# Performance work log

Hardware: AMD Instinct MI355X
Metric: run time of the kernel (lower is better)

## Reference

```python
import jax, jax.numpy as jnp
from jax import lax
import numpy as np

STEP = 0.1            # step_size
INC = 1.5             # bracket_expansion_increase
MAX_EXPAND = 16       # fixed cap on bracket-expansion iterations (masked no-ops after convergence)
MAX_SHRINK = 24       # fixed cap on shrinkage-rejection iterations


def setup_inputs() -> dict:
    key = jax.random.key(0)
    kx, kw = jax.random.split(key)
    B, D = 65536, 128
    x = jax.random.normal(kx, (B, D), jnp.float32)
    W = jax.random.normal(kw, (D, D), jnp.float32) / np.float32(np.sqrt(D))
    return {"x": x, "W": W}


def _potential(x, W):
    # correlated Gaussian potential: -0.5 * ||W x||^2, per chain
    z = x @ W.T                      # [B, D]
    return -0.5 * jnp.sum(z * z, axis=-1)  # [B]


def _slice_sample(x, W):
    B = x.shape[0]
    key = jax.random.key(42)
    k_y, k_dir, k_u0, k_shr = jax.random.split(key, 4)

    pot = _potential(x, W)                               # [B]
    # y = log(1 - u) + potential  (log of uniform height under the density)
    y = jnp.log1p(-jax.random.uniform(k_y, pot.shape, jnp.float32)) + pot

    dirs = jax.random.normal(k_dir, x.shape, jnp.float32)
    dirs = dirs / jnp.linalg.norm(dirs, axis=-1, keepdims=True)  # unit slice directions

    mask0 = y < pot

    # --- bracket expansion (lower: sign=-1, upper: sign=+1), masked fixed-trip scan ---
    def expand(sign):
        def body(carry, i):
            b, mask = carry
            step_i = STEP * jnp.power(jnp.float32(INC), i.astype(jnp.float32))
            b = jnp.where(mask, b + sign * step_i, b)
            pot_b = _potential(x + b[:, None] * dirs, W)
            mask = mask & (y < pot_b)
            return (b, mask), None
        (b, _), _ = lax.scan(body, (jnp.zeros((B,), jnp.float32), mask0),
                             jnp.arange(MAX_EXPAND))
        return b

    lb = expand(-1.0)
    ub = expand(+1.0)

    # --- initial proposal on the bracket ---
    u = jax.random.uniform(k_u0, (B,), jnp.float32) * (ub - lb) + lb
    x_new = x + u[:, None] * dirs
    mask = _potential(x_new, W) < y   # rejected chains

    # --- shrinkage loop (masked fixed-trip scan) ---
    def shrink(carry, k):
        u, lb, ub, x_new, mask = carry
        smaller = u < 0
        lb = jnp.where(mask & smaller, u, lb)
        ub = jnp.where(mask & ~smaller, u, ub)
        u_prop = jax.random.uniform(k, (B,), jnp.float32) * (ub - lb) + lb
        u = jnp.where(mask, u_prop, u)
        cand = x + u[:, None] * dirs
        pot_c = _potential(cand, W)
        x_new = jnp.where(mask[:, None], cand, x_new)
        mask = mask & (pot_c < y)
        return (u, lb, ub, x_new, mask), None

    keys = jax.random.split(k_shr, MAX_SHRINK)
    (u, lb, ub, x_new, mask), _ = lax.scan(shrink, (u, lb, ub, x_new, mask), keys)
    return x_new


def reference(x, W):
    return _slice_sample(x, W)
```

## Files before the change

kernel.cpp:

```cpp
#include <hip/hip_runtime.h>
#include <stdint.h>
#include <math.h>


#define BD 128
#define NB 65536
#define WS 132
#define XDS 130

typedef float f32x2 __attribute__((ext_vector_type(2)));
typedef struct { f32x2 lo, hi; } f32x2x2;

#define PK_FMA_LO(acc, xd, wp) \
  asm("v_pk_fma_f32 %0, %1, %2, %0 op_sel_hi:[1,0,1]" \
      : "+v"(acc) : "v"(xd), "v"(wp))
#define PK_FMA_HI(acc, xd, wp) \
  asm("v_pk_fma_f32 %0, %1, %2, %0 op_sel:[0,1,0] op_sel_hi:[1,1,1]" \
      : "+v"(acc) : "v"(xd), "v"(wp))

__host__ __device__ inline uint32_t rotl32(uint32_t v, int s) {
  return (v << s) | (v >> (32 - s));
}

__host__ __device__ inline void tf2x32(uint32_t k0, uint32_t k1,
                                       uint32_t c0, uint32_t c1,
                                       uint32_t* o0, uint32_t* o1) {
  uint32_t ks2 = k0 ^ k1 ^ 0x1BD11BDAu;
  uint32_t x0 = c0 + k0, x1 = c1 + k1;
#define TFR(r) x0 += x1; x1 = rotl32(x1, (r)); x1 ^= x0;
  TFR(13) TFR(15) TFR(26) TFR(6)
  x0 += k1;  x1 += ks2 + 1u;
  TFR(17) TFR(29) TFR(16) TFR(24)
  x0 += ks2; x1 += k0 + 2u;
  TFR(13) TFR(15) TFR(26) TFR(6)
  x0 += k0;  x1 += k1 + 3u;
  TFR(17) TFR(29) TFR(16) TFR(24)
  x0 += k1;  x1 += ks2 + 4u;
  TFR(13) TFR(15) TFR(26) TFR(6)
  x0 += ks2; x1 += k0 + 5u;
#undef TFR
  *o0 = x0; *o1 = x1;
}

__device__ inline uint32_t jbits(uint32_t k0, uint32_t k1, uint32_t n) {
  uint32_t a, b;
  tf2x32(k0, k1, 0u, n, &a, &b);
  return a ^ b;
}

__device__ inline float u01(uint32_t bits) {
  return __fsub_rn(__uint_as_float((bits >> 9) | 0x3f800000u), 1.0f);
}

__device__ inline float xla_log1p(float x) {
  float u  = __fadd_rn(x, 1.0f);
  float lg = (float)log((double)u);
  float sm = __fmul_rn(__fadd_rn(__fmul_rn(-0.5f, x), 1.0f), x);
  return (fabsf(x) < 1e-4f) ? sm : lg;
}

__device__ inline float xla_erfinv(float x) {
  float xx = __fmul_rn(x, x);
  float w  = -xla_log1p(-xx);
  float p;
  if (w < 5.0f) {
    float ww = __fsub_rn(w, 2.5f);
    p = 2.81022636e-08f;
    p = __fadd_rn(3.43273939e-07f,  __fmul_rn(p, ww));
    p = __fadd_rn(-3.5233877e-06f,  __fmul_rn(p, ww));
    p = __fadd_rn(-4.39150654e-06f, __fmul_rn(p, ww));
    p = __fadd_rn(0.00021858087f,   __fmul_rn(p, ww));
    p = __fadd_rn(-0.00125372503f,  __fmul_rn(p, ww));
    p = __fadd_rn(-0.00417768164f,  __fmul_rn(p, ww));
    p = __fadd_rn(0.246640727f,     __fmul_rn(p, ww));
    p = __fadd_rn(1.50140941f,      __fmul_rn(p, ww));
  } else {
    float ww = __fsub_rn(__fsqrt_rn(w), 3.0f);
    p = -0.000200214257f;
    p = __fadd_rn(0.000100950558f,  __fmul_rn(p, ww));
    p = __fadd_rn(0.00134934322f,   __fmul_rn(p, ww));
    p = __fadd_rn(-0.00367342844f,  __fmul_rn(p, ww));
    p = __fadd_rn(0.00573950773f,   __fmul_rn(p, ww));
    p = __fadd_rn(-0.0076224613f,   __fmul_rn(p, ww));
    p = __fadd_rn(0.00943887047f,   __fmul_rn(p, ww));
    p = __fadd_rn(1.00167406f,      __fmul_rn(p, ww));
    p = __fadd_rn(2.83297682f,      __fmul_rn(p, ww));
  }
  return __fmul_rn(p, x);
}

__device__ __attribute__((always_inline)) inline float potential16(
    const f32x2* __restrict__ xdr, const float* __restrict__ wr, float coef) {
  float z[8] = {0.f, 0.f, 0.f, 0.f, 0.f, 0.f, 0.f, 0.f};
#pragma unroll 2
  for (int q = 0; q < 32; ++q) {
    float4 p01 = *(const float4*)(xdr + q * 4);
    float4 p23 = *(const float4*)(xdr + q * 4 + 2);
    float c0 = __fadd_rn(p01.x, __fmul_rn(coef, p01.y));
    float c1 = __fadd_rn(p01.z, __fmul_rn(coef, p01.w));
    float c2 = __fadd_rn(p23.x, __fmul_rn(coef, p23.y));
    float c3 = __fadd_rn(p23.z, __fmul_rn(coef, p23.w));
#pragma unroll
    for (int m = 0; m < 8; ++m) {
      float4 wv = *(const float4*)(wr + m * (16 * WS) + q * 4);
      z[m] = __fmaf_rn(c0, wv.x, z[m]);
      z[m] = __fmaf_rn(c1, wv.y, z[m]);
      z[m] = __fmaf_rn(c2, wv.z, z[m]);
      z[m] = __fmaf_rn(c3, wv.w, z[m]);
    }
  }
  float pr = 0.0f;
#pragma unroll
  for (int m = 0; m < 8; ++m) pr = __fadd_rn(pr, __fmul_rn(z[m], z[m]));
#pragma unroll
  for (int msk = 32; msk >= 4; msk >>= 1)
    pr = __fadd_rn(pr, __shfl_xor(pr, msk));
  return __fmul_rn(-0.5f, pr);
}

__device__ inline double epsb(float u) {
  double au = fabs((double)u);
  return 4e-4 + 8e-5 * au + 8e-6 * au * au;
}

struct KeyArgs {
  uint32_t ky0, ky1;
  uint32_t ku0, ku1;
  uint32_t kd0, kd1;
  uint32_t ksh0, ksh1;
};

__global__ __launch_bounds__(1024, 1) void slice_fused_kernel(
    const float* __restrict__ X, const float* __restrict__ Wg,
    float* __restrict__ OUT, KeyArgs ka) {
  __shared__ __align__(16) float Wl[128 * WS];
  __shared__ __align__(16) f32x2 XDl[64 * XDS];

  const int tid   = threadIdx.x;
  const int cbase = blockIdx.x * 64;

  for (int i = tid; i < 128 * 32; i += 1024) {
    int r = i >> 5, q = i & 31;
    *(float4*)&Wl[r * WS + q * 4] = ((const float4*)Wg)[i];
  }
  for (int i = tid; i < 64 * 32; i += 1024) {
    int cc = i >> 5, q = i & 31;
    float4 xv = ((const float4*)(X + (size_t)(cbase + cc) * BD))[q];
    float* b0 = (float*)&XDl[cc * XDS + q * 4];
    b0[0] = xv.x; b0[2] = xv.y; b0[4] = xv.z; b0[6] = xv.w;
  }

  const int wave = tid >> 6, lane = tid & 63;
  const int c    = lane & 3;
  const int j    = lane >> 2;
  const int cl   = wave * 4 + c;
  const uint32_t chain = (uint32_t)(cbase + cl);

  float uA, uB;
  {
    uint32_t a0, a1;
    tf2x32(ka.ksh0, ka.ksh1, 0u, (uint32_t)j, &a0, &a1);
    uA = u01(jbits(a0, a1, chain));
    uint32_t d0, d1;
    tf2x32(ka.ksh0, ka.ksh1, 0u, 16u + (uint32_t)j, &d0, &d1);
    uint32_t bk0 = (j < 8) ? d0 : (j == 8 ? ka.ky0 : ka.ku0);
    uint32_t bk1 = (j < 8) ? d1 : (j == 8 ? ka.ky1 : ka.ku1);
    uB = u01(jbits(bk0, bk1, chain));
  }

  {
    const float LO    = __uint_as_float(0xBF7FFFFFu);
    const float SQRT2 = __uint_as_float(0x3FB504F3u);
    float vm[8];
#pragma unroll
    for (int m = 0; m < 8; ++m) {
      uint32_t n = chain * 128u + (uint32_t)(16 * m + j);
      float f  = u01(jbits(ka.kd0, ka.kd1, n));
      float um = fmaxf(LO, __fadd_rn(__fmul_rn(f, 2.0f), LO));
      vm[m] = __fmul_rn(SQRT2, xla_erfinv(um));
    }
    float pr = 0.0f;
#pragma unroll
    for (int m = 0; m < 8; ++m) pr = __fadd_rn(pr, __fmul_rn(vm[m], vm[m]));
#pragma unroll
    for (int msk = 32; msk >= 4; msk >>= 1)
      pr = __fadd_rn(pr, __shfl_xor(pr, msk));
    float nrm = __fsqrt_rn(pr);
#pragma unroll
    for (int m = 0; m < 8; ++m)
      ((float*)&XDl[cl * XDS + 16 * m + j])[1] = vm[m] / nrm;
  }

  __syncthreads();

  const f32x2* xdr = &XDl[cl * XDS];
  const float* wr  = &Wl[j * WS];

  f32x2 zab[8];
#pragma unroll
  for (int m = 0; m < 8; ++m) zab[m] = (f32x2){0.0f, 0.0f};
#pragma unroll 2
  for (int q = 0; q < 32; ++q) {
    f32x2x2 P0 = *(const f32x2x2*)(xdr + q * 4);
    f32x2x2 P1 = *(const f32x2x2*)(xdr + q * 4 + 2);
#pragma unroll
    for (int m = 0; m < 8; ++m) {
      const f32x2x2 wq = *(const f32x2x2*)(wr + m * (16 * WS) + q * 4);
      PK_FMA_LO(zab[m], P0.lo, wq.lo);
      PK_FMA_HI(zab[m], P0.hi, wq.lo);
      PK_FMA_LO(zab[m], P1.lo, wq.hi);
      PK_FMA_HI(zab[m], P1.hi, wq.hi);
    }
  }

  float pr0 = 0.0f;
#pragma unroll
  for (int m = 0; m < 8; ++m) pr0 = __fadd_rn(pr0, __fmul_rn(zab[m].x, zab[m].x));
#pragma unroll
  for (int msk = 32; msk >= 4; msk >>= 1)
    pr0 = __fadd_rn(pr0, __shfl_xor(pr0, msk));
  float pot0 = __fmul_rn(-0.5f, pr0);

  double gl = 0.0, hl = 0.0;
#pragma unroll
  for (int m = 0; m < 8; ++m) {
    gl += (double)zab[m].x * (double)zab[m].y;
    hl += (double)zab[m].y * (double)zab[m].y;
  }
#pragma unroll
  for (int msk = 32; msk >= 4; msk >>= 1) {
    gl += __shfl_xor(gl, msk);
    hl += __shfl_xor(hl, msk);
  }
  const double g = gl, h = hl;
  const double potd0 = (double)pot0;

  float Uy = __shfl(uB, c + 32);
  float y  = __fadd_rn(xla_log1p(-Uy), pot0);
  const double yd = (double)y;
  bool mask0 = (y < pot0);

  float lb = 0.0f, ub = 0.0f;
#pragma unroll 1
  for (int side = 0; side < 2; ++side) {
    bool m = mask0;
    float b = 0.0f, pw = 1.0f;
#pragma unroll 1
    for (int i = 0; i < 16; ++i) {
      if (!__any((int)m)) break;
      float step = __fmul_rn(0.1f, pw);
      pw = __fmul_rn(pw, 1.5f);
      if (m) b = side ? __fadd_rn(b, step) : __fsub_rn(b, step);
      double bd   = (double)b;
      double diff = (potd0 - bd * g - 0.5 * bd * bd * h) - yd;
      bool need = m && (fabs(diff) <= epsb(b));
      float pe = 0.0f;
      if (__any((int)need)) pe = potential16(xdr, wr, b);
      bool cont = need ? (y < pe) : (diff > 0.0);
      m = m && cont;
    }
    if (side == 0) lb = b; else ub = b;
  }

  float U0 = __shfl(uB, c + 36);
  float u  = __fadd_rn(__fmul_rn(U0, __fsub_rn(ub, lb)), lb);
  bool rej;
  {
    double ud   = (double)u;
    double diff = (potd0 - ud * g - 0.5 * ud * ud * h) - yd;
    bool need = fabs(diff) <= epsb(u);
    float pe = 0.0f;
    if (__any((int)need)) pe = potential16(xdr, wr, u);
    rej = need ? (pe < y) : (diff < 0.0);
  }

#pragma unroll 1
  for (int t = 0; t < 24; ++t) {
    if (!__any((int)rej)) break;
    float Ut = (t < 16) ? __shfl(uA, c + 4 * t) : __shfl(uB, c + 4 * (t - 16));
    if (rej) {
      if (u < 0.0f) lb = u; else ub = u;
      u = __fadd_rn(__fmul_rn(Ut, __fsub_rn(ub, lb)), lb);
    }
    double ud   = (double)u;
    double diff = (potd0 - ud * g - 0.5 * ud * ud * h) - yd;
    bool need = rej && (fabs(diff) <= epsb(u));
    float pe = 0.0f;
    if (__any((int)need)) pe = potential16(xdr, wr, u);
    bool rj = need ? (pe < y) : (diff < 0.0);
    rej = rej && rj;
  }

  float* orow = OUT + (size_t)chain * BD;
#pragma unroll
  for (int hh = 0; hh < 2; ++hh) {
    int q2 = j * 2 + hh;
    float4 p01 = *(const float4*)(xdr + q2 * 4);
    float4 p23 = *(const float4*)(xdr + q2 * 4 + 2);
    float4 o;
    o.x = __fadd_rn(p01.x, __fmul_rn(u, p01.y));
    o.y = __fadd_rn(p01.z, __fmul_rn(u, p01.w));
    o.z = __fadd_rn(p23.x, __fmul_rn(u, p23.y));
    o.w = __fadd_rn(p23.z, __fmul_rn(u, p23.w));
    *(float4*)&orow[q2 * 4] = o;
  }
}

extern "C" void kernel_launch(void* const* d_in, const int* in_sizes, int n_in,
                              void* d_out, int out_size, void* d_ws, size_t ws_size,
                              hipStream_t stream) {
  (void)in_sizes; (void)n_in; (void)d_ws; (void)ws_size; (void)out_size;
  const float* x = (const float*)d_in[0];
  const float* W = (const float*)d_in[1];
  float* out = (float*)d_out;

  const uint32_t R0 = 0u, R1 = 42u;
  KeyArgs ka;
  tf2x32(R0, R1, 0u, 0u, &ka.ky0, &ka.ky1);
  tf2x32(R0, R1, 0u, 1u, &ka.kd0, &ka.kd1);
  tf2x32(R0, R1, 0u, 2u, &ka.ku0, &ka.ku1);
  tf2x32(R0, R1, 0u, 3u, &ka.ksh0, &ka.ksh1);

  slice_fused_kernel<<<dim3(NB / 64), dim3(1024), 0, stream>>>(x, W, out, ka);
}
```

Baseline: 140.5 us.

## Drop LDS x/direction buffer, stage direction in output buffer, raise occupancy hint

Removes the shared-memory buffer that held interleaved x and direction rows. x is now read straight from global memory, and the unit direction is written into the output row and read back from there. Later the same row is overwritten with the final sample. This halves LDS use so more blocks can be resident per CU, and the launch-bounds occupancy hint is raised from 1 to 8. The cost is that the matvec and every potential evaluation now load x and direction through the global/L1 path instead of LDS. The stronger occupancy hint may also force register caps and spills.

```diff
diff --git a/kernel.cpp b/kernel.cpp
--- a/kernel.cpp
+++ b/kernel.cpp
@@ -6,7 +6,6 @@
 #define BD 128
 #define NB 65536
 #define WS 132
-#define XDS 130
 
 typedef float f32x2 __attribute__((ext_vector_type(2)));
 typedef struct { f32x2 lo, hi; } f32x2x2;
@@ -90,16 +89,17 @@
 }
 
 __device__ __attribute__((always_inline)) inline float potential16(
-    const f32x2* __restrict__ xdr, const float* __restrict__ wr, float coef) {
+    const float* __restrict__ xrow, const float* __restrict__ drow,
+    const float* __restrict__ wr, float coef) {
   float z[8] = {0.f, 0.f, 0.f, 0.f, 0.f, 0.f, 0.f, 0.f};
 #pragma unroll 2
   for (int q = 0; q < 32; ++q) {
-    float4 p01 = *(const float4*)(xdr + q * 4);
-    float4 p23 = *(const float4*)(xdr + q * 4 + 2);
-    float c0 = __fadd_rn(p01.x, __fmul_rn(coef, p01.y));
-    float c1 = __fadd_rn(p01.z, __fmul_rn(coef, p01.w));
-    float c2 = __fadd_rn(p23.x, __fmul_rn(coef, p23.y));
-    float c3 = __fadd_rn(p23.z, __fmul_rn(coef, p23.w));
+    float4 xq = *(const float4*)(xrow + q * 4);
+    float4 dq = *(const float4*)(drow + q * 4);
+    float c0 = __fadd_rn(xq.x, __fmul_rn(coef, dq.x));
+    float c1 = __fadd_rn(xq.y, __fmul_rn(coef, dq.y));
+    float c2 = __fadd_rn(xq.z, __fmul_rn(coef, dq.z));
+    float c3 = __fadd_rn(xq.w, __fmul_rn(coef, dq.w));
 #pragma unroll
     for (int m = 0; m < 8; ++m) {
       float4 wv = *(const float4*)(wr + m * (16 * WS) + q * 4);
@@ -130,11 +130,10 @@
   uint32_t ksh0, ksh1;
 };
 
-__global__ __launch_bounds__(1024, 1) void slice_fused_kernel(
+__global__ __launch_bounds__(1024, 8) void slice_fused_kernel(
     const float* __restrict__ X, const float* __restrict__ Wg,
     float* __restrict__ OUT, KeyArgs ka) {
   __shared__ __align__(16) float Wl[128 * WS];
-  __shared__ __align__(16) f32x2 XDl[64 * XDS];
 
   const int tid   = threadIdx.x;
   const int cbase = blockIdx.x * 64;
@@ -142,12 +141,6 @@
   for (int i = tid; i < 128 * 32; i += 1024) {
     int r = i >> 5, q = i & 31;
     *(float4*)&Wl[r * WS + q * 4] = ((const float4*)Wg)[i];
-  }
-  for (int i = tid; i < 64 * 32; i += 1024) {
-    int cc = i >> 5, q = i & 31;
-    float4 xv = ((const float4*)(X + (size_t)(cbase + cc) * BD))[q];
-    float* b0 = (float*)&XDl[cc * XDS + q * 4];
-    b0[0] = xv.x; b0[2] = xv.y; b0[4] = xv.z; b0[6] = xv.w;
   }
 
   const int wave = tid >> 6, lane = tid & 63;
@@ -155,6 +148,9 @@
   const int j    = lane >> 2;
   const int cl   = wave * 4 + c;
   const uint32_t chain = (uint32_t)(cbase + cl);
+
+  const float* xrow = X   + (size_t)chain * BD;
+  float*       drow = OUT + (size_t)chain * BD;
 
   float uA, uB;
   {
@@ -188,28 +184,29 @@
     float nrm = __fsqrt_rn(pr);
 #pragma unroll
     for (int m = 0; m < 8; ++m)
-      ((float*)&XDl[cl * XDS + 16 * m + j])[1] = vm[m] / nrm;
+      drow[16 * m + j] = vm[m] / nrm;
   }
 
   __syncthreads();
 
-  const f32x2* xdr = &XDl[cl * XDS];
-  const float* wr  = &Wl[j * WS];
+  const float* wr = &Wl[j * WS];
 
   f32x2 zab[8];
 #pragma unroll
   for (int m = 0; m < 8; ++m) zab[m] = (f32x2){0.0f, 0.0f};
 #pragma unroll 2
   for (int q = 0; q < 32; ++q) {
-    f32x2x2 P0 = *(const f32x2x2*)(xdr + q * 4);
-    f32x2x2 P1 = *(const f32x2x2*)(xdr + q * 4 + 2);
+    float4 xq = *(const float4*)(xrow + q * 4);
+    float4 dq = *(const float4*)(drow + q * 4);
+    f32x2 xd0 = {xq.x, dq.x}, xd1 = {xq.y, dq.y};
+    f32x2 xd2 = {xq.z, dq.z}, xd3 = {xq.w, dq.w};
 #pragma unroll
     for (int m = 0; m < 8; ++m) {
       const f32x2x2 wq = *(const f32x2x2*)(wr + m * (16 * WS) + q * 4);
-      PK_FMA_LO(zab[m], P0.lo, wq.lo);
-      PK_FMA_HI(zab[m], P0.hi, wq.lo);
-      PK_FMA_LO(zab[m], P1.lo, wq.hi);
-      PK_FMA_HI(zab[m], P1.hi, wq.hi);
+      PK_FMA_LO(zab[m], xd0, wq.lo);
+      PK_FMA_HI(zab[m], xd1, wq.lo);
+      PK_FMA_LO(zab[m], xd2, wq.hi);
+      PK_FMA_HI(zab[m], xd3, wq.hi);
     }
   }
 
@@ -255,7 +252,7 @@
       double diff = (potd0 - bd * g - 0.5 * bd * bd * h) - yd;
       bool need = m && (fabs(diff) <= epsb(b));
       float pe = 0.0f;
-      if (__any((int)need)) pe = potential16(xdr, wr, b);
+      if (__any((int)need)) pe = potential16(xrow, drow, wr, b);
       bool cont = need ? (y < pe) : (diff > 0.0);
       m = m && cont;
     }
@@ -270,7 +267,7 @@
     double diff = (potd0 - ud * g - 0.5 * ud * ud * h) - yd;
     bool need = fabs(diff) <= epsb(u);
     float pe = 0.0f;
-    if (__any((int)need)) pe = potential16(xdr, wr, u);
+    if (__any((int)need)) pe = potential16(xrow, drow, wr, u);
     rej = need ? (pe < y) : (diff < 0.0);
   }
 
@@ -286,23 +283,22 @@
     double diff = (potd0 - ud * g - 0.5 * ud * ud * h) - yd;
     bool need = rej && (fabs(diff) <= epsb(u));
     float pe = 0.0f;
-    if (__any((int)need)) pe = potential16(xdr, wr, u);
+    if (__any((int)need)) pe = potential16(xrow, drow, wr, u);
     bool rj = need ? (pe < y) : (diff < 0.0);
     rej = rej && rj;
   }
 
-  float* orow = OUT + (size_t)chain * BD;
 #pragma unroll
   for (int hh = 0; hh < 2; ++hh) {
     int q2 = j * 2 + hh;
-    float4 p01 = *(const float4*)(xdr + q2 * 4);
-    float4 p23 = *(const float4*)(xdr + q2 * 4 + 2);
+    float4 xq = *(const float4*)(xrow + q2 * 4);
+    float4 dq = *(const float4*)(drow + q2 * 4);
     float4 o;
-    o.x = __fadd_rn(p01.x, __fmul_rn(u, p01.y));
-    o.y = __fadd_rn(p01.z, __fmul_rn(u, p01.w));
-    o.z = __fadd_rn(p23.x, __fmul_rn(u, p23.y));
-    o.w = __fadd_rn(p23.z, __fmul_rn(u, p23.w));
-    *(float4*)&orow[q2 * 4] = o;
+    o.x = __fadd_rn(xq.x, __fmul_rn(u, dq.x));
+    o.y = __fadd_rn(xq.y, __fmul_rn(u, dq.y));
+    o.z = __fadd_rn(xq.z, __fmul_rn(u, dq.z));
+    o.w = __fadd_rn(xq.w, __fmul_rn(u, dq.w));
+    *(float4*)(drow + q2 * 4) = o;
   }
 }
 
```

Measured after the change: 197.9 us. 40.9% more time.
